# Kernel tuning notes

Measured on AMD Instinct MI355X. Metric: run time of the kernel, lower is better.

The kernel has to match this reference:

```python
import jax, jax.numpy as jnp
import numpy as np

G = 8            # group_order
KS = 3           # kernel size
C1, O1 = 1, 16   # gconv1 channels
C2, O2 = 16, 32  # gconv2 channels
HW = 28
NUM_CLASSES = 10


def _bilinear_sample(img, px, py):
    # img: (O, I, K, K); px, py: (K, K) pixel coords; zero padding outside
    # (matches torch grid_sample bilinear, align_corners=False, padding_mode='zeros')
    K = img.shape[-1]
    x0 = jnp.floor(px); y0 = jnp.floor(py)
    wx = px - x0; wy = py - y0
    x0i = x0.astype(jnp.int32); y0i = y0.astype(jnp.int32)

    def gather(yi, xi):
        valid = (yi >= 0) & (yi < K) & (xi >= 0) & (xi < K)
        yc = jnp.clip(yi, 0, K - 1)
        xc = jnp.clip(xi, 0, K - 1)
        return img[:, :, yc, xc] * valid.astype(img.dtype)  # (O,I,K,K)

    return (gather(y0i, x0i) * (1 - wx) * (1 - wy)
            + gather(y0i, x0i + 1) * wx * (1 - wy)
            + gather(y0i + 1, x0i) * (1 - wx) * wy
            + gather(y0i + 1, x0i + 1) * wx * wy)


def _rotated_kernels(base, group_order):
    # Replicates F.affine_grid + F.grid_sample (align_corners=False) for each rotation k.
    K = base.shape[-1]
    coords = (2.0 * jnp.arange(K, dtype=base.dtype) + 1.0) / K - 1.0  # normalized centers
    xs, ys = jnp.meshgrid(coords, coords, indexing='xy')  # x along width, y along height

    def rot_k(k):
        theta = 2.0 * np.pi * k / group_order
        c, s = jnp.cos(theta), jnp.sin(theta)
        gx = c * xs - s * ys   # theta row [cos, -sin, 0]
        gy = s * xs + c * ys   # theta row [sin,  cos, 0]
        px = ((gx + 1.0) * K - 1.0) / 2.0  # unnormalize, align_corners=False
        py = ((gy + 1.0) * K - 1.0) / 2.0
        return _bilinear_sample(base, px, py)

    return jax.vmap(rot_k)(jnp.arange(group_order, dtype=base.dtype))  # (G,O,I,K,K)


def _conv2d(x, w, pad):
    return jax.lax.conv_general_dilated(
        x, w, window_strides=(1, 1), padding=[(pad, pad), (pad, pad)],
        dimension_numbers=('NCHW', 'OIHW', 'NCHW'))


def setup_inputs() -> dict:
    key = jax.random.key(0)
    k1, k2, k3, k4, k5 = jax.random.split(key, 5)
    x = jax.random.normal(k1, (512, C1, HW, HW), dtype=jnp.float32)
    base_weight = jax.random.normal(k2, (O1, C1, KS, KS), dtype=jnp.float32)
    w2 = jax.random.normal(k3, (O2, C2, G, KS, KS), dtype=jnp.float32) * 0.05
    fc_w = jax.random.normal(k4, (NUM_CLASSES, O2 * HW * HW), dtype=jnp.float32) * 0.01
    fc_b = jax.random.normal(k5, (NUM_CLASSES,), dtype=jnp.float32) * 0.01
    return {"x": x, "base_weight": base_weight, "w2": w2, "fc_w": fc_w, "fc_b": fc_b}


def reference(x, base_weight, w2, fc_w, fc_b):
    B = x.shape[0]
    # --- GroupConv2D: steerable rotated kernels, concat along out-channels (k-major) ---
    rk = _rotated_kernels(base_weight, G)           # (G, O1, C1, K, K)
    w1 = rk.reshape(G * O1, C1, KS, KS)
    h = _conv2d(x, w1, 1)                           # (B, G*O1, 28, 28)
    h = jax.nn.relu(h)                              # GroupReLU == plain ReLU

    # --- GroupToGroupConv: circulant structure fused into one conv ---
    # torch: out channel = g*O2 + o (cat dim=1), in channel = c*G + h_idx (view layout)
    g = jnp.arange(G)[:, None]
    hh = jnp.arange(G)[None, :]
    idx = (g - hh) % G                               # (G, G)
    Wc = w2[:, :, idx]                               # (O2, C2, G_g, G_h, K, K)
    Wbig = jnp.transpose(Wc, (2, 0, 1, 3, 4, 5)).reshape(G * O2, C2 * G, KS, KS)
    h2 = _conv2d(h, Wbig, 1)                         # (B, G*O2, 28, 28)
    h2 = jax.nn.relu(h2)

    # --- GroupPooling (mean over the *inner* factor of 8, as in the torch view) ---
    p = h2.reshape(B, (G * O2) // G, G, HW, HW).mean(axis=2)  # (B, 32, 28, 28)

    # --- fc ---
    flat = p.reshape(B, -1)
    return flat @ fc_w.T + fc_b
```

## Files before the change

### kernel.cpp

```cpp
#include <hip/hip_runtime.h>
#include <hip/hip_bf16.h>
#include <cstdint>

#define AS1 __attribute__((address_space(1)))
#define AS3 __attribute__((address_space(3)))

typedef __bf16 bf16x8 __attribute__((ext_vector_type(8)));
typedef float  f32x16 __attribute__((ext_vector_type(16)));

__device__ __forceinline__ void gld_lds16(const void* g, void* l) {
    __builtin_amdgcn_global_load_lds((const AS1 void*)g, (AS3 void*)l, 16, 0, 0);
}

__global__ __launch_bounds__(256) void k_conv1(const float* __restrict__ x,
                                               const float* __restrict__ base,
                                               const float* __restrict__ w2,
                                               __hip_bfloat16* __restrict__ hl,
                                               __hip_bfloat16* __restrict__ A) {
    int tid = threadIdx.x;

    if (blockIdx.x < 1152) {
        int i = blockIdx.x * 256 + tid;
        int r = i / 1152, k = i - r * 1152;
        int g = r >> 5, o2 = r & 31;
        int kk = k >> 7, cch = k & 127;
        int ky = kk / 3, kx = kk - ky * 3;
        int c2 = cch >> 3, hh = cch & 7;
        int gi = (g - hh) & 7;
        A[i] = __float2bfloat16(w2[((o2 * 16 + c2) * 8 + gi) * 9 + ky * 3 + kx]);
    }

    __shared__ float w1s[1152];
    if (tid < 128) {
        int g = tid >> 4, o = tid & 15;
        float th = 6.28318530717958647692f * (float)g / 8.0f;
        float c = cosf(th), s = sinf(th);
        for (int i = 0; i < 3; ++i) {
            float ys = (2.0f * i + 1.0f) / 3.0f - 1.0f;
            for (int j = 0; j < 3; ++j) {
                float xs = (2.0f * j + 1.0f) / 3.0f - 1.0f;
                float gx = c * xs - s * ys;
                float gy = s * xs + c * ys;
                float px = ((gx + 1.0f) * 3.0f - 1.0f) * 0.5f;
                float py = ((gy + 1.0f) * 3.0f - 1.0f) * 0.5f;
                float x0 = floorf(px), y0 = floorf(py);
                float wx = px - x0, wy = py - y0;
                int x0i = (int)x0, y0i = (int)y0;
                auto gat = [&](int yi, int xi) -> float {
                    bool v = (yi >= 0) && (yi < 3) && (xi >= 0) && (xi < 3);
                    int yc = min(max(yi, 0), 2), xc = min(max(xi, 0), 2);
                    return v ? base[o * 9 + yc * 3 + xc] : 0.0f;
                };
                w1s[tid * 9 + i * 3 + j] =
                      gat(y0i, x0i)         * (1.0f - wx) * (1.0f - wy)
                    + gat(y0i, x0i + 1)     * wx          * (1.0f - wy)
                    + gat(y0i + 1, x0i)     * (1.0f - wx) * wy
                    + gat(y0i + 1, x0i + 1) * wx          * wy;
            }
        }
    }
    __syncthreads();

    const int c0 = (tid & 15) * 8;
    float wreg[8][9];
#pragma unroll
    for (int cc = 0; cc < 8; ++cc)
#pragma unroll
        for (int k = 0; k < 9; ++k) wreg[cc][k] = w1s[(c0 + cc) * 9 + k];

    const int ps = tid >> 4;
    const int pbase = blockIdx.x * 64;

#pragma unroll
    for (int j = 0; j < 4; ++j) {
        int pi = pbase + j * 16 + ps;
        int xx = pi % 30; int t = pi / 30; int yy = t % 30; int b = t / 30;
        float acc[8] = {0.f,0.f,0.f,0.f,0.f,0.f,0.f,0.f};
        if (xx >= 1 && xx <= 28 && yy >= 1 && yy <= 28) {
            const float* xb = x + b * 784;
            int y = yy - 1, xc = xx - 1;
#pragma unroll
            for (int dy = -1; dy <= 1; ++dy) {
                int sy = y + dy;
#pragma unroll
                for (int dx = -1; dx <= 1; ++dx) {
                    int sx = xc + dx;
                    float xv = (sy >= 0 && sy < 28 && sx >= 0 && sx < 28) ? xb[sy * 28 + sx] : 0.0f;
                    int k = (dy + 1) * 3 + (dx + 1);
#pragma unroll
                    for (int cc = 0; cc < 8; ++cc) acc[cc] += xv * wreg[cc][k];
                }
            }
        }
        union { __hip_bfloat16 h[8]; float4 f4; } u;
#pragma unroll
        for (int cc = 0; cc < 8; ++cc) u.h[cc] = __float2bfloat16(fmaxf(acc[cc], 0.0f));
        *(float4*)(hl + (size_t)pi * 128 + c0) = u.f4;
    }
}

__global__ __launch_bounds__(256) void k_conv2(const __hip_bfloat16* __restrict__ A,
                                               const __hip_bfloat16* __restrict__ hl,
                                               float* __restrict__ p) {
    __shared__ __align__(16) char smem[32768];

    const int tid  = threadIdx.x;
    const int lane = tid & 63;
    const int w    = tid >> 6;
    const int wr   = w >> 1, wc = w & 1;
    const int hi   = lane >> 5;

    const int bid  = blockIdx.x;
    const int xcd  = bid & 7;
    const int slot = bid >> 3;
    const int nt   = xcd + 8 * (slot >> 1);
    const int mt   = slot & 1;
    const int n0 = nt << 7;
    const int r0 = mt << 7;

    uint32_t aG[4], bG[4], ldsOff[4];
#pragma unroll
    for (int q = 0; q < 4; ++q) {
        int ch = w * 4 + q;
        int rl = ch * 8 + (lane >> 3);
        int ca = (lane & 7) ^ (rl & 7);
        aG[q] = (uint32_t)((r0 + rl) * 2304 + ca * 16);
        int n  = n0 + rl;
        int b  = n / 784; int rr = n - b * 784;
        int y  = rr / 28; int xx = rr - y * 28;
        bG[q]  = (uint32_t)(((b * 30 + y) * 30 + xx) * 256 + ca * 16);
        ldsOff[q] = (uint32_t)(ch * 1024);
    }

    uint32_t aro[2], bro[2]; int asw[2], bsw[2];
#pragma unroll
    for (int t = 0; t < 2; ++t) {
        int rl = 64 * wr + 32 * t + (lane & 31);
        aro[t] = (uint32_t)(rl * 128); asw[t] = rl & 7;
        int nl = 64 * wc + 32 * t + (lane & 31);
        bro[t] = (uint32_t)(16384 + nl * 128); bsw[t] = nl & 7;
    }

    f32x16 acc[2][2];
#pragma unroll
    for (int i = 0; i < 2; ++i)
#pragma unroll
        for (int j = 0; j < 2; ++j) acc[i][j] = (f32x16)(0.0f);

    const char* Ab = (const char*)A;
    const char* Hb = (const char*)hl;

    for (int s = 0; s < 18; ++s) {
        int kk = s >> 1, half = s & 1;
        int ky = kk / 3, kx = kk - ky * 3;
        int aoff = kk * 256 + half * 128;
        int boff = (ky * 30 + kx) * 256 + half * 128;

        __syncthreads();
#pragma unroll
        for (int q = 0; q < 4; ++q) {
            gld_lds16(Ab + aG[q] + aoff, smem + ldsOff[q]);
            gld_lds16(Hb + bG[q] + boff, smem + 16384 + ldsOff[q]);
        }
        __syncthreads();

#pragma unroll
        for (int kstep = 0; kstep < 4; ++kstep) {
            int cb = kstep * 2 + hi;
            bf16x8 af[2], bf[2];
#pragma unroll
            for (int t = 0; t < 2; ++t) {
                af[t] = *(const bf16x8*)(smem + aro[t] + ((cb ^ asw[t]) * 16));
                bf[t] = *(const bf16x8*)(smem + bro[t] + ((cb ^ bsw[t]) * 16));
            }
#pragma unroll
            for (int i = 0; i < 2; ++i)
#pragma unroll
                for (int j = 0; j < 2; ++j)
                    acc[i][j] = __builtin_amdgcn_mfma_f32_32x32x16_bf16(af[i], bf[j], acc[i][j], 0, 0, 0);
        }
    }

#pragma unroll
    for (int ti = 0; ti < 2; ++ti) {
        int gbase = (r0 + 64 * wr + 32 * ti) >> 3;
#pragma unroll
        for (int tj = 0; tj < 2; ++tj) {
            f32x16 v = acc[ti][tj];
#pragma unroll
            for (int q = 0; q < 4; ++q) {
                float s = fmaxf(v[4*q], 0.0f) + fmaxf(v[4*q+1], 0.0f)
                        + fmaxf(v[4*q+2], 0.0f) + fmaxf(v[4*q+3], 0.0f);
                s += __shfl_xor(s, 32, 64);
                if (hi == 0) {
                    int a = gbase + q;
                    int n = n0 + 64 * wc + 32 * tj + (lane & 31);
                    int b = n / 784; int rr = n - b * 784;
                    p[(b * 32 + a) * 784 + rr] = s * 0.125f;
                }
            }
        }
    }
}

__global__ __launch_bounds__(256) void k_fc(const float* __restrict__ p,
                                            const float* __restrict__ fw,
                                            const float* __restrict__ fb,
                                            float* __restrict__ out) {
    int b = blockIdx.x >> 2, ks = blockIdx.x & 3;
    int tid = threadIdx.x;
    const float4* p4 = (const float4*)(p + (size_t)b * 25088);
    const float4* w4 = (const float4*)fw;
    float acc[10] = {};
    for (int i = ks * 1568 + tid; i < (ks + 1) * 1568; i += 256) {
        float4 v = p4[i];
#pragma unroll
        for (int c = 0; c < 10; ++c) {
            float4 u = w4[c * 6272 + i];
            acc[c] += v.x * u.x + v.y * u.y + v.z * u.z + v.w * u.w;
        }
    }
    __shared__ float red[10][4];
    int lane = tid & 63, wv = tid >> 6;
#pragma unroll
    for (int c = 0; c < 10; ++c) {
        float s = acc[c];
#pragma unroll
        for (int o = 32; o > 0; o >>= 1) s += __shfl_down(s, o, 64);
        if (lane == 0) red[c][wv] = s;
    }
    __syncthreads();
    if (tid < 10) {
        float s = red[tid][0] + red[tid][1] + red[tid][2] + red[tid][3];
        if (ks == 0) s += fb[tid];
        atomicAdd(&out[b * 10 + tid], s);
    }
}

extern "C" void kernel_launch(void* const* d_in, const int* in_sizes, int n_in,
                              void* d_out, int out_size, void* d_ws, size_t ws_size,
                              hipStream_t stream) {
    const float* x  = (const float*)d_in[0];
    const float* bw = (const float*)d_in[1];
    const float* w2 = (const float*)d_in[2];
    const float* fw = (const float*)d_in[3];
    const float* fb = (const float*)d_in[4];
    float* out = (float*)d_out;
    char* ws = (char*)d_ws;

    __hip_bfloat16* Amat = (__hip_bfloat16*)(ws + 4608);
    __hip_bfloat16* hl   = (__hip_bfloat16*)(ws + 594432);
    float*          p    = (float*)(ws + 118563328);

    hipMemsetAsync(d_out, 0, (size_t)out_size * sizeof(float), stream);
    k_conv1<<<7200, 256, 0, stream>>>(x, bw, w2, hl, Amat);
    k_conv2<<<6272, 256, 0, stream>>>(Amat, hl, p);
    k_fc   <<<2048, 256, 0, stream>>>(p, fw, fb, out);
}
```

Measured before the change: 396.5 us.

## Store pooled activations in bf16, stage FC weights in LDS, extend conv2 swizzle

Result: no change. 392.4 us (-1.0%).

```diff
diff --git a/kernel.cpp b/kernel.cpp
--- a/kernel.cpp
+++ b/kernel.cpp
@@ -101,7 +101,7 @@
 
 __global__ __launch_bounds__(256) void k_conv2(const __hip_bfloat16* __restrict__ A,
                                                const __hip_bfloat16* __restrict__ hl,
-                                               float* __restrict__ p) {
+                                               __hip_bfloat16* __restrict__ p) {
     __shared__ __align__(16) char smem[32768];
 
     const int tid  = threadIdx.x;
@@ -123,7 +123,7 @@
     for (int q = 0; q < 4; ++q) {
         int ch = w * 4 + q;
         int rl = ch * 8 + (lane >> 3);
-        int ca = (lane & 7) ^ (rl & 7);
+        int ca = (lane & 7) ^ (rl & 7) ^ (ch & 3);
         aG[q] = (uint32_t)((r0 + rl) * 2304 + ca * 16);
         int n  = n0 + rl;
         int b  = n / 784; int rr = n - b * 784;
@@ -136,9 +136,9 @@
 #pragma unroll
     for (int t = 0; t < 2; ++t) {
         int rl = 64 * wr + 32 * t + (lane & 31);
-        aro[t] = (uint32_t)(rl * 128); asw[t] = rl & 7;
+        aro[t] = (uint32_t)(rl * 128); asw[t] = (rl & 7) ^ ((rl >> 3) & 3);
         int nl = 64 * wc + 32 * t + (lane & 31);
-        bro[t] = (uint32_t)(16384 + nl * 128); bsw[t] = nl & 7;
+        bro[t] = (uint32_t)(16384 + nl * 128); bsw[t] = (nl & 7) ^ ((nl >> 3) & 3);
     }
 
     f32x16 acc[2][2];
@@ -196,44 +196,57 @@
                     int a = gbase + q;
                     int n = n0 + 64 * wc + 32 * tj + (lane & 31);
                     int b = n / 784; int rr = n - b * 784;
-                    p[(b * 32 + a) * 784 + rr] = s * 0.125f;
+                    p[(b * 32 + a) * 784 + rr] = __float2bfloat16(s * 0.125f);
                 }
             }
         }
     }
 }
 
-__global__ __launch_bounds__(256) void k_fc(const float* __restrict__ p,
+__global__ __launch_bounds__(256) void k_fc(const __hip_bfloat16* __restrict__ p,
                                             const float* __restrict__ fw,
                                             const float* __restrict__ fb,
                                             float* __restrict__ out) {
-    int b = blockIdx.x >> 2, ks = blockIdx.x & 3;
-    int tid = threadIdx.x;
-    const float4* p4 = (const float4*)(p + (size_t)b * 25088);
+    __shared__ float4 wl[3920];
+    const int bb = blockIdx.x >> 4;
+    const int ks = blockIdx.x & 15;
+    const int tid = threadIdx.x;
     const float4* w4 = (const float4*)fw;
+    for (int i = tid; i < 3920; i += 256) {
+        int c = i / 392, j = i - c * 392;
+        wl[i] = w4[c * 6272 + ks * 392 + j];
+    }
+    __syncthreads();
+
+    const int kl = tid & 15, bi = tid >> 4;
+    const int b = bb * 16 + bi;
+    const bf16x8* pb = (const bf16x8*)(p + (size_t)b * 25088 + ks * 1568);
     float acc[10] = {};
-    for (int i = ks * 1568 + tid; i < (ks + 1) * 1568; i += 256) {
-        float4 v = p4[i];
+    for (int t = kl; t < 196; t += 16) {
+        union { bf16x8 v; __hip_bfloat16 h[8]; } u;
+        u.v = pb[t];
+        float vf[8];
+#pragma unroll
+        for (int e = 0; e < 8; ++e) vf[e] = __bfloat162float(u.h[e]);
 #pragma unroll
         for (int c = 0; c < 10; ++c) {
-            float4 u = w4[c * 6272 + i];
-            acc[c] += v.x * u.x + v.y * u.y + v.z * u.z + v.w * u.w;
-        }
-    }
-    __shared__ float red[10][4];
-    int lane = tid & 63, wv = tid >> 6;
+            float4 u0 = wl[c * 392 + 2 * t];
+            float4 u1 = wl[c * 392 + 2 * t + 1];
+            acc[c] += vf[0] * u0.x + vf[1] * u0.y + vf[2] * u0.z + vf[3] * u0.w
+                    + vf[4] * u1.x + vf[5] * u1.y + vf[6] * u1.z + vf[7] * u1.w;
+        }
+    }
 #pragma unroll
     for (int c = 0; c < 10; ++c) {
         float s = acc[c];
-#pragma unroll
-        for (int o = 32; o > 0; o >>= 1) s += __shfl_down(s, o, 64);
-        if (lane == 0) red[c][wv] = s;
-    }
-    __syncthreads();
-    if (tid < 10) {
-        float s = red[tid][0] + red[tid][1] + red[tid][2] + red[tid][3];
-        if (ks == 0) s += fb[tid];
-        atomicAdd(&out[b * 10 + tid], s);
+        s += __shfl_down(s, 8, 16);
+        s += __shfl_down(s, 4, 16);
+        s += __shfl_down(s, 2, 16);
+        s += __shfl_down(s, 1, 16);
+        if (kl == 0) {
+            if (ks == 0) s += fb[c];
+            atomicAdd(&out[b * 10 + c], s);
+        }
     }
 }
 
@@ -250,10 +263,10 @@
 
     __hip_bfloat16* Amat = (__hip_bfloat16*)(ws + 4608);
     __hip_bfloat16* hl   = (__hip_bfloat16*)(ws + 594432);
-    float*          p    = (float*)(ws + 118563328);
+    __hip_bfloat16* p    = (__hip_bfloat16*)(ws + 118563328);
 
     hipMemsetAsync(d_out, 0, (size_t)out_size * sizeof(float), stream);
     k_conv1<<<7200, 256, 0, stream>>>(x, bw, w2, hl, Amat);
     k_conv2<<<6272, 256, 0, stream>>>(Amat, hl, p);
-    k_fc   <<<2048, 256, 0, stream>>>(p, fw, fb, out);
-}
+    k_fc   <<<512,  256, 0, stream>>>(p, fw, fb, out);
+}
```

## Fuse FC layer into conv2 epilogue and adjust LDS swizzle pattern

Applied to the files above, without the earlier changes.

Measured after the change: 602.1 us. 51.9% more time.

```diff
diff --git a/kernel.cpp b/kernel.cpp
--- a/kernel.cpp
+++ b/kernel.cpp
@@ -101,8 +101,11 @@
 
 __global__ __launch_bounds__(256) void k_conv2(const __hip_bfloat16* __restrict__ A,
                                                const __hip_bfloat16* __restrict__ hl,
-                                               float* __restrict__ p) {
+                                               const float* __restrict__ fw,
+                                               const float* __restrict__ fb,
+                                               float* __restrict__ out) {
     __shared__ __align__(16) char smem[32768];
+    __shared__ float fcp[2][10];
 
     const int tid  = threadIdx.x;
     const int lane = tid & 63;
@@ -123,7 +126,7 @@
     for (int q = 0; q < 4; ++q) {
         int ch = w * 4 + q;
         int rl = ch * 8 + (lane >> 3);
-        int ca = (lane & 7) ^ (rl & 7);
+        int ca = (lane & 7) ^ (rl & 7) ^ (ch & 3);
         aG[q] = (uint32_t)((r0 + rl) * 2304 + ca * 16);
         int n  = n0 + rl;
         int b  = n / 784; int rr = n - b * 784;
@@ -136,9 +139,9 @@
 #pragma unroll
     for (int t = 0; t < 2; ++t) {
         int rl = 64 * wr + 32 * t + (lane & 31);
-        aro[t] = (uint32_t)(rl * 128); asw[t] = rl & 7;
+        aro[t] = (uint32_t)(rl * 128); asw[t] = (rl & 7) ^ ((rl >> 3) & 3);
         int nl = 64 * wc + 32 * t + (lane & 31);
-        bro[t] = (uint32_t)(16384 + nl * 128); bsw[t] = nl & 7;
+        bro[t] = (uint32_t)(16384 + nl * 128); bsw[t] = (nl & 7) ^ ((nl >> 3) & 3);
     }
 
     f32x16 acc[2][2];
@@ -181,6 +184,17 @@
         }
     }
 
+    float accfc[2][10];
+    int bb_[2], rr_[2];
+#pragma unroll
+    for (int tj = 0; tj < 2; ++tj) {
+#pragma unroll
+        for (int c = 0; c < 10; ++c) accfc[tj][c] = 0.0f;
+        int n = n0 + 64 * wc + 32 * tj + (lane & 31);
+        int b = n / 784;
+        bb_[tj] = b; rr_[tj] = n - b * 784;
+    }
+    const int qlo = hi * 2;
 #pragma unroll
     for (int ti = 0; ti < 2; ++ti) {
         int gbase = (r0 + 64 * wr + 32 * ti) >> 3;
@@ -192,48 +206,38 @@
                 float s = fmaxf(v[4*q], 0.0f) + fmaxf(v[4*q+1], 0.0f)
                         + fmaxf(v[4*q+2], 0.0f) + fmaxf(v[4*q+3], 0.0f);
                 s += __shfl_xor(s, 32, 64);
-                if (hi == 0) {
+                if (q >= qlo && q < qlo + 2) {
+                    float sp = s * 0.125f;
                     int a = gbase + q;
-                    int n = n0 + 64 * wc + 32 * tj + (lane & 31);
-                    int b = n / 784; int rr = n - b * 784;
-                    p[(b * 32 + a) * 784 + rr] = s * 0.125f;
+                    const float* fwp = fw + a * 784 + rr_[tj];
+#pragma unroll
+                    for (int c = 0; c < 10; ++c)
+                        accfc[tj][c] += sp * fwp[c * 25088];
                 }
             }
         }
     }
-}
-
-__global__ __launch_bounds__(256) void k_fc(const float* __restrict__ p,
-                                            const float* __restrict__ fw,
-                                            const float* __restrict__ fb,
-                                            float* __restrict__ out) {
-    int b = blockIdx.x >> 2, ks = blockIdx.x & 3;
-    int tid = threadIdx.x;
-    const float4* p4 = (const float4*)(p + (size_t)b * 25088);
-    const float4* w4 = (const float4*)fw;
-    float acc[10] = {};
-    for (int i = ks * 1568 + tid; i < (ks + 1) * 1568; i += 256) {
-        float4 v = p4[i];
-#pragma unroll
-        for (int c = 0; c < 10; ++c) {
-            float4 u = w4[c * 6272 + i];
-            acc[c] += v.x * u.x + v.y * u.y + v.z * u.z + v.w * u.w;
-        }
-    }
-    __shared__ float red[10][4];
-    int lane = tid & 63, wv = tid >> 6;
-#pragma unroll
-    for (int c = 0; c < 10; ++c) {
-        float s = acc[c];
-#pragma unroll
-        for (int o = 32; o > 0; o >>= 1) s += __shfl_down(s, o, 64);
-        if (lane == 0) red[c][wv] = s;
-    }
-    __syncthreads();
-    if (tid < 10) {
-        float s = red[tid][0] + red[tid][1] + red[tid][2] + red[tid][3];
-        if (ks == 0) s += fb[tid];
-        atomicAdd(&out[b * 10 + tid], s);
+
+    __syncthreads();
+    if (tid < 20) ((float*)fcp)[tid] = 0.0f;
+    __syncthreads();
+    const int b0 = n0 / 784;
+#pragma unroll
+    for (int tj = 0; tj < 2; ++tj) {
+        int idx = bb_[tj] - b0;
+#pragma unroll
+        for (int c = 0; c < 10; ++c)
+            atomicAdd(&fcp[idx][c], accfc[tj][c]);
+    }
+    __syncthreads();
+    if (tid < 20) {
+        int idx = tid / 10, c = tid - idx * 10;
+        int b = b0 + idx;
+        if (b < 512) {
+            float s = fcp[idx][c];
+            if (mt == 0 && b * 784 >= n0 && b * 784 < n0 + 128) s += fb[c];
+            atomicAdd(&out[b * 10 + c], s);
+        }
     }
 }
 
@@ -250,10 +254,8 @@
 
     __hip_bfloat16* Amat = (__hip_bfloat16*)(ws + 4608);
     __hip_bfloat16* hl   = (__hip_bfloat16*)(ws + 594432);
-    float*          p    = (float*)(ws + 118563328);
 
     hipMemsetAsync(d_out, 0, (size_t)out_size * sizeof(float), stream);
     k_conv1<<<7200, 256, 0, stream>>>(x, bw, w2, hl, Amat);
-    k_conv2<<<6272, 256, 0, stream>>>(Amat, hl, p);
-    k_fc   <<<2048, 256, 0, stream>>>(p, fw, fb, out);
-}
+    k_conv2<<<6272, 256, 0, stream>>>(Amat, hl, fw, fb, out);
+}
```
